# Kernel tuning notes

Hardware: AMD Instinct MI355X
Metric: run time of the kernel (lower is better)

The kernel has to match this reference:

```python
import jax, jax.numpy as jnp
import numpy as np

N_HEADS_ROUTER = 8
N_HEADS_INPUT = 4
LN_EPS = 1e-5

def gelu(x):
    return jax.nn.gelu(x, approximate=False)  # torch F.gelu default (erf)

def mha(x, wq, wk, wv, bq, bk, bv, wo, bo, n_heads):
    # PyTorch nn.MultiheadAttention (batch_first, eval mode)
    B, S, E = x.shape
    d = E // n_heads
    scale = 1.0 / np.sqrt(d).astype(np.float32)
    def split(t):
        return t.reshape(B, S, n_heads, d).transpose(0, 2, 1, 3)  # [B,H,S,d]
    q = split(x @ wq.T + bq)
    k = split(x @ wk.T + bk)
    v = split(x @ wv.T + bv)
    attn = jax.nn.softmax(jnp.einsum('bhqd,bhkd->bhqk', q, k) * scale, axis=-1)
    o = jnp.einsum('bhqk,bhkd->bhqd', attn, v).transpose(0, 2, 1, 3).reshape(B, S, E)
    return o @ wo.T + bo

def layer_norm(x, g, b):
    mu = x.mean(axis=-1, keepdims=True)
    var = ((x - mu) ** 2).mean(axis=-1, keepdims=True)
    return (x - mu) * jax.lax.rsqrt(var + LN_EPS) * g + b

def setup_inputs() -> dict:
    key = jax.random.key(0)
    ks = jax.random.split(key, 20)
    B, S, D, NI, NP = 4, 1024, 1024, 512, 1024
    def rn(k, shape, s=0.02):
        return jax.random.normal(k, shape, jnp.float32) * s
    return {
        'x': jax.random.normal(ks[0], (B, S, D), jnp.float32),
        # DynamicRouter MHA (embed=d_model, 8 heads)
        'r_wq': rn(ks[1], (D, D)), 'r_wk': rn(ks[2], (D, D)), 'r_wv': rn(ks[3], (D, D)),
        'r_bq': jnp.zeros((D,), jnp.float32), 'r_bk': jnp.zeros((D,), jnp.float32), 'r_bv': jnp.zeros((D,), jnp.float32),
        'r_wo': rn(ks[4], (D, D)), 'r_bo': jnp.zeros((D,), jnp.float32),
        'aff_w': rn(ks[5], (NI, D)), 'aff_b': jnp.zeros((NI,), jnp.float32),
        # InputNeurons
        'patterns': rn(ks[6], (NI, D), 0.05),
        'i_wq': rn(ks[7], (NI, NI)), 'i_wk': rn(ks[8], (NI, NI)), 'i_wv': rn(ks[9], (NI, NI)),
        'i_bq': jnp.zeros((NI,), jnp.float32), 'i_bk': jnp.zeros((NI,), jnp.float32), 'i_bv': jnp.zeros((NI,), jnp.float32),
        'i_wo': rn(ks[10], (NI, NI)), 'i_bo': jnp.zeros((NI,), jnp.float32),
        'ln_g': jnp.ones((NI,), jnp.float32), 'ln_b': jnp.zeros((NI,), jnp.float32),
        # ProcessNeurons
        'comb_w': rn(ks[11], (NP, NI), 0.05),
        'proj_w': rn(ks[12], (NP, D), 0.05),
        'k_input': 256,
        'k_process': 512,
    }

def reference(x, r_wq, r_wk, r_wv, r_bq, r_bk, r_bv, r_wo, r_bo, aff_w, aff_b,
              patterns, i_wq, i_wk, i_wv, i_bq, i_bk, i_bv, i_wo, i_bo,
              ln_g, ln_b, comb_w, proj_w, k_input, k_process):
    B, S, D = x.shape
    NI = aff_w.shape[0]
    # --- DynamicRouter ---
    context = mha(x, r_wq, r_wk, r_wv, r_bq, r_bk, r_bv, r_wo, r_bo, N_HEADS_ROUTER)
    affinity = context @ aff_w.T + aff_b           # [B,S,NI]
    scores = affinity.max(axis=1)                  # [B,NI] (max-pool over seq)
    probs = jax.nn.softmax(scores, axis=-1)
    _, idx = jax.lax.top_k(scores, k_input)        # [B,k_in]
    one_hot = jax.nn.one_hot(idx, NI, dtype=probs.dtype).sum(axis=1)  # [B,NI]
    weights = jax.lax.stop_gradient(one_hot - probs) + probs          # straight-through
    # --- InputNeurons ---
    act = gelu(context @ patterns.T)               # [B,S,NI]
    attn_out = mha(act, i_wq, i_wk, i_wv, i_bq, i_bk, i_bv, i_wo, i_bo, N_HEADS_INPUT)
    act = layer_norm(act + attn_out, ln_g, ln_b)
    # --- select input neurons ---
    weighted = act * weights[:, None, :]
    sel = jnp.take_along_axis(weighted, jnp.broadcast_to(idx[:, None, :], (B, S, k_input)), axis=2)  # [B,S,k_in]
    # --- ProcessNeurons ---
    sel_w = comb_w[:, idx].transpose(1, 0, 2)      # [B, NP, k_in]
    pa = gelu(jnp.einsum('bsk,bpk->bsp', sel, sel_w))  # [B,S,NP]
    ps = pa.mean(axis=1)                            # [B,NP]
    _, pidx = jax.lax.top_k(ps, k_process)          # [B,k_p]
    spa = jnp.take_along_axis(pa, jnp.broadcast_to(pidx[:, None, :], (B, S, k_process)), axis=2)  # [B,S,k_p]
    sproj = proj_w[pidx]                            # [B,k_p,D]
    return jnp.einsum('bsk,bkd->bsd', spa, sproj)   # [B,S,D]
```

## Files before the change

kernel.cpp:

```cpp
#include <hip/hip_runtime.h>
#include <math.h>

#define DEVI static __device__ __forceinline__

typedef __attribute__((ext_vector_type(8))) short short8;
typedef __attribute__((ext_vector_type(4))) float f32x4;
typedef unsigned short u16;

DEVI float gelu_f(float x) {
    return 0.5f * x * (1.0f + erff(x * 0.7071067811865475f));
}
DEVI u16 f2bf(float f) {
    unsigned u = __builtin_bit_cast(unsigned, f);
    return (u16)((u + 0x7fffu + ((u >> 16) & 1u)) >> 16);
}
DEVI float bf2f(u16 b) {
    unsigned u = ((unsigned)b) << 16;
    return __builtin_bit_cast(float, u);
}
DEVI void split_bf(float v, u16& h, u16& l) {
    h = f2bf(v);
    l = f2bf(v - bf2f(h));
}

template<int BN, bool SPLIT, bool DO_GELU, int OMODE>
__global__ __launch_bounds__(256, 2)
void gemm_planes(const u16* __restrict__ Agh, const u16* __restrict__ Agl,
                 const u16* __restrict__ Bgh, const u16* __restrict__ Bgl,
                 const float* __restrict__ bias, float* __restrict__ Cf,
                 u16* __restrict__ O1h, u16* __restrict__ O1l,
                 u16* __restrict__ O2h, u16* __restrict__ O2l,
                 u16* __restrict__ O3h, u16* __restrict__ O3l,
                 int M, int N, int K, int HH, int partN)
{
    constexpr int BM = 128, BK = 64, PK = 72;
    constexpr int NPL = SPLIT ? 2 : 1;
    constexpr int MF  = (BN == 128) ? 4 : 2;
    constexpr int NB  = BN / 32;
    __shared__ __align__(16) u16 As[NPL][BM * PK];
    __shared__ __align__(16) u16 Bs[NPL][BN * PK];
    const int t = threadIdx.x, w = t >> 6, l = t & 63;
    const int lr = l & 15, lg = l >> 4;
    const int m0 = blockIdx.y * BM, n0 = blockIdx.x * BN;
    const int moff = (BN == 128) ? (w >> 1) * 64 : w * 32;
    const int noff = (BN == 128) ? (w & 1) * 64 : 0;
    const int srow = t >> 3, sslot = t & 7;

    f32x4 acc[MF][4];
    #pragma unroll
    for (int i = 0; i < MF; ++i)
        #pragma unroll
        for (int j = 0; j < 4; ++j) acc[i][j] = 0.0f;

    for (int k0 = 0; k0 < K; k0 += BK) {
        __syncthreads();
        #pragma unroll
        for (int p = 0; p < 4; ++p) {
            int row = p * 32 + srow;
            size_t g = (size_t)(m0 + row) * K + k0 + sslot * 8;
            *(uint4*)&As[0][row * PK + sslot * 8] = *(const uint4*)&Agh[g];
            if constexpr (SPLIT)
                *(uint4*)&As[1][row * PK + sslot * 8] = *(const uint4*)&Agl[g];
        }
        #pragma unroll
        for (int p = 0; p < NB; ++p) {
            int row = p * 32 + srow;
            size_t g = (size_t)(n0 + row) * K + k0 + sslot * 8;
            *(uint4*)&Bs[0][row * PK + sslot * 8] = *(const uint4*)&Bgh[g];
            if constexpr (SPLIT)
                *(uint4*)&Bs[1][row * PK + sslot * 8] = *(const uint4*)&Bgl[g];
        }
        __syncthreads();
        #pragma unroll
        for (int ks = 0; ks < 2; ++ks) {
            short8 af[MF][NPL], bfr[4][NPL];
            #pragma unroll
            for (int mf = 0; mf < MF; ++mf) {
                int a = (moff + mf * 16 + lr) * PK + ks * 32 + lg * 8;
                af[mf][0] = *(const short8*)&As[0][a];
                if constexpr (SPLIT) af[mf][1] = *(const short8*)&As[1][a];
            }
            #pragma unroll
            for (int nf = 0; nf < 4; ++nf) {
                int a = (noff + nf * 16 + lr) * PK + ks * 32 + lg * 8;
                bfr[nf][0] = *(const short8*)&Bs[0][a];
                if constexpr (SPLIT) bfr[nf][1] = *(const short8*)&Bs[1][a];
            }
            #pragma unroll
            for (int mf = 0; mf < MF; ++mf)
                #pragma unroll
                for (int nf = 0; nf < 4; ++nf) {
                    acc[mf][nf] = __builtin_amdgcn_mfma_f32_16x16x32_bf16(
                        af[mf][0], bfr[nf][0], acc[mf][nf], 0, 0, 0);
                    if constexpr (SPLIT) {
                        acc[mf][nf] = __builtin_amdgcn_mfma_f32_16x16x32_bf16(
                            af[mf][0], bfr[nf][1], acc[mf][nf], 0, 0, 0);
                        acc[mf][nf] = __builtin_amdgcn_mfma_f32_16x16x32_bf16(
                            af[mf][1], bfr[nf][0], acc[mf][nf], 0, 0, 0);
                    }
                }
        }
    }

    float colred[4];
    if constexpr (OMODE == 4) {
        colred[0] = colred[1] = colred[2] = colred[3] = -3.402823466e38f;
    } else if constexpr (OMODE == 5) {
        colred[0] = colred[1] = colred[2] = colred[3] = 0.0f;
    }
    #pragma unroll
    for (int mf = 0; mf < MF; ++mf)
        #pragma unroll
        for (int nf = 0; nf < 4; ++nf) {
            int col  = n0 + noff + nf * 16 + lr;
            int mrow = m0 + moff + mf * 16 + lg * 4;
            float bv = bias ? bias[col] : 0.0f;
            float ov[4];
            #pragma unroll
            for (int r = 0; r < 4; ++r) ov[r] = acc[mf][nf][r] + bv;
            if constexpr (OMODE == 0) {
                #pragma unroll
                for (int r = 0; r < 4; ++r) {
                    float o = ov[r];
                    if constexpr (DO_GELU) o = gelu_f(o);
                    Cf[(size_t)(mrow + r) * N + col] = o;
                }
            } else if constexpr (OMODE == 1) {
                #pragma unroll
                for (int r = 0; r < 4; ++r) {
                    float o = ov[r];
                    if constexpr (DO_GELU) o = gelu_f(o);
                    u16 hb, lb; split_bf(o, hb, lb);
                    O1h[(size_t)(mrow + r) * N + col] = hb;
                    O1l[(size_t)(mrow + r) * N + col] = lb;
                }
            } else if constexpr (OMODE == 3) {
                if (col < partN) {
                    #pragma unroll
                    for (int r = 0; r < 4; ++r) {
                        u16 hb, lb; split_bf(ov[r], hb, lb);
                        O1h[(size_t)(mrow + r) * partN + col] = hb;
                        O1l[(size_t)(mrow + r) * partN + col] = lb;
                    }
                } else if (col < 2 * partN) {
                    int c2 = col - partN;
                    #pragma unroll
                    for (int r = 0; r < 4; ++r) {
                        u16 hb, lb; split_bf(ov[r], hb, lb);
                        O2h[(size_t)(mrow + r) * partN + c2] = hb;
                        O2l[(size_t)(mrow + r) * partN + c2] = lb;
                    }
                } else {
                    int c2 = col - 2 * partN;
                    int hh = c2 >> 7, dd = c2 & 127;
                    int bb = mrow >> 10, s0 = mrow & 1023;
                    size_t idx = ((size_t)(bb * HH + hh) * 128 + dd) * 1024 + s0;
                    ushort4 oh, ol;
                    #pragma unroll
                    for (int r = 0; r < 4; ++r) {
                        u16 hb, lb; split_bf(ov[r], hb, lb);
                        ((u16*)&oh)[r] = hb; ((u16*)&ol)[r] = lb;
                    }
                    *(ushort4*)&O3h[idx] = oh;
                    *(ushort4*)&O3l[idx] = ol;
                }
            } else if constexpr (OMODE == 4) {
                if (n0 < partN) {
                    #pragma unroll
                    for (int r = 0; r < 4; ++r)
                        colred[nf] = fmaxf(colred[nf], ov[r]);
                } else {
                    int c2 = col - partN;
                    #pragma unroll
                    for (int r = 0; r < 4; ++r) {
                        float o = gelu_f(ov[r]);
                        u16 hb, lb; split_bf(o, hb, lb);
                        O1h[(size_t)(mrow + r) * partN + c2] = hb;
                        O1l[(size_t)(mrow + r) * partN + c2] = lb;
                    }
                }
            } else if constexpr (OMODE == 5) {
                #pragma unroll
                for (int r = 0; r < 4; ++r) {
                    float o = gelu_f(ov[r]);
                    colred[nf] += o;
                    u16 hb, lb; split_bf(o, hb, lb);
                    O1h[(size_t)(mrow + r) * N + col] = hb;
                    O1l[(size_t)(mrow + r) * N + col] = lb;
                }
            }
        }
    if constexpr (OMODE == 4 || OMODE == 5) {
        bool doRed = (OMODE == 5) || (n0 < partN);
        if (doRed) {
            __syncthreads();
            float* sred = (float*)&As[0][0];
            #pragma unroll
            for (int nf = 0; nf < 4; ++nf) sred[t * 4 + nf] = colred[nf];
            __syncthreads();
            if (t < 128) {
                int cl = t, lrr = cl & 15, nff = (cl & 63) >> 4, wb = cl >> 6;
                float a = (OMODE == 4) ? -3.402823466e38f : 0.0f;
                #pragma unroll
                for (int k2 = 0; k2 < 2; ++k2)
                    #pragma unroll
                    for (int l2 = 0; l2 < 4; ++l2) {
                        float v = sred[(((wb + 2 * k2) * 64) + l2 * 16 + lrr) * 4 + nff];
                        if constexpr (OMODE == 4) a = fmaxf(a, v); else a += v;
                    }
                int stride = (OMODE == 4) ? partN : N;
                Cf[(size_t)blockIdx.y * stride + n0 + cl] = a;
            }
        }
    }
}

__global__ __launch_bounds__(256, 3)
void attn_planes(const u16* __restrict__ Qh, const u16* __restrict__ Ql,
                 const u16* __restrict__ Kh, const u16* __restrict__ Kl,
                 const u16* __restrict__ Vh, const u16* __restrict__ Vl,
                 u16* __restrict__ Oh, u16* __restrict__ Ol,
                 int S, int Dm, int H, float scale)
{
    __shared__ __align__(16) u16 KsL[2][32 * 136];
    __shared__ __align__(16) u16 VsL[2][128 * 40];
    __shared__ __align__(16) u16 PsL[2][4 * 16 * 40];
    const int t = threadIdx.x, w = t >> 6, l = t & 63;
    const int lr = l & 15, lg = l >> 4;
    const int nqt = gridDim.x;
    const int nwg = nqt * gridDim.y;
    const int fid = blockIdx.y * nqt + blockIdx.x;
    const int nid = (fid & 7) * (nwg >> 3) + (fid >> 3);
    const int bh = nid / nqt, qt = nid - bh * nqt;
    const int b = bh / H, h = bh - b * H;
    const int q0 = qt * 64 + w * 16;
    const size_t qkbase = (size_t)(b * S) * Dm + h * 128;
    const size_t vbase  = (size_t)(b * H + h) * 128 * 1024;

    short8 qhf[4], qlf[4];
    #pragma unroll
    for (int ks = 0; ks < 4; ++ks) {
        size_t g = qkbase + (size_t)(q0 + lr) * Dm + ks * 32 + lg * 8;
        qhf[ks] = *(const short8*)&Qh[g];
        qlf[ks] = *(const short8*)&Ql[g];
    }
    f32x4 accO[8];
    #pragma unroll
    for (int i = 0; i < 8; ++i) accO[i] = 0.0f;
    float ls = 0.0f;
    const int pw = w * 640;

    for (int c0 = 0; c0 < S; c0 += 32) {
        __syncthreads();
        #pragma unroll
        for (int p = 0; p < 2; ++p) {
            int key = p * 16 + (t >> 4);
            int slot = t & 15;
            size_t g = qkbase + (size_t)(c0 + key) * Dm + slot * 8;
            *(uint4*)&KsL[0][key * 136 + slot * 8] = *(const uint4*)&Kh[g];
            *(uint4*)&KsL[1][key * 136 + slot * 8] = *(const uint4*)&Kl[g];
        }
        #pragma unroll
        for (int p = 0; p < 2; ++p) {
            int d = p * 64 + (t >> 2);
            int ksl = t & 3;
            size_t g = vbase + (size_t)d * 1024 + c0 + ksl * 8;
            *(uint4*)&VsL[0][d * 40 + ksl * 8] = *(const uint4*)&Vh[g];
            *(uint4*)&VsL[1][d * 40 + ksl * 8] = *(const uint4*)&Vl[g];
        }
        __syncthreads();
        f32x4 sac[2];
        sac[0] = 0.0f; sac[1] = 0.0f;
        #pragma unroll
        for (int mt = 0; mt < 2; ++mt)
            #pragma unroll
            for (int ks = 0; ks < 4; ++ks) {
                int a = (mt * 16 + lr) * 136 + ks * 32 + lg * 8;
                short8 khf = *(const short8*)&KsL[0][a];
                short8 klf = *(const short8*)&KsL[1][a];
                sac[mt] = __builtin_amdgcn_mfma_f32_16x16x32_bf16(khf, qhf[ks], sac[mt], 0, 0, 0);
                sac[mt] = __builtin_amdgcn_mfma_f32_16x16x32_bf16(khf, qlf[ks], sac[mt], 0, 0, 0);
                sac[mt] = __builtin_amdgcn_mfma_f32_16x16x32_bf16(klf, qhf[ks], sac[mt], 0, 0, 0);
            }
        #pragma unroll
        for (int mt = 0; mt < 2; ++mt)
            #pragma unroll
            for (int rr = 0; rr < 4; ++rr) {
                float p = __expf(sac[mt][rr] * scale);
                ls += p;
                int key = mt * 16 + lg * 4 + rr;
                u16 hb, lb; split_bf(p, hb, lb);
                PsL[0][pw + lr * 40 + key] = hb;
                PsL[1][pw + lr * 40 + key] = lb;
            }
        short8 pah = *(const short8*)&PsL[0][pw + lr * 40 + lg * 8];
        short8 pal = *(const short8*)&PsL[1][pw + lr * 40 + lg * 8];
        #pragma unroll
        for (int nt = 0; nt < 8; ++nt) {
            int a = (nt * 16 + lr) * 40 + lg * 8;
            short8 vhf = *(const short8*)&VsL[0][a];
            short8 vlf = *(const short8*)&VsL[1][a];
            accO[nt] = __builtin_amdgcn_mfma_f32_16x16x32_bf16(pah, vhf, accO[nt], 0, 0, 0);
            accO[nt] = __builtin_amdgcn_mfma_f32_16x16x32_bf16(pah, vlf, accO[nt], 0, 0, 0);
            accO[nt] = __builtin_amdgcn_mfma_f32_16x16x32_bf16(pal, vhf, accO[nt], 0, 0, 0);
        }
    }
    float lt = ls + __shfl_xor(ls, 16, 64);
    lt += __shfl_xor(lt, 32, 64);
    #pragma unroll
    for (int rr = 0; rr < 4; ++rr) {
        float inv = 1.0f / __shfl(lt, lg * 4 + rr, 64);
        size_t rowoff = qkbase + (size_t)(q0 + lg * 4 + rr) * Dm;
        #pragma unroll
        for (int nt = 0; nt < 8; ++nt) {
            float o = accO[nt][rr] * inv;
            u16 hb, lb; split_bf(o, hb, lb);
            Oh[rowoff + nt * 16 + lr] = hb;
            Ol[rowoff + nt * 16 + lr] = lb;
        }
    }
}

struct PSeg { const float* s; u16* h; u16* l; int n4; int pad; };
struct PArgs { PSeg g[8]; };

__global__ __launch_bounds__(256)
void pack_many(PArgs a)
{
    PSeg sg = a.g[blockIdx.y];
    int i = blockIdx.x * 256 + threadIdx.x;
    if (i >= sg.n4) return;
    float4 v = *(const float4*)&sg.s[i * 4];
    ushort4 hv, lv;
    split_bf(v.x, hv.x, lv.x);
    split_bf(v.y, hv.y, lv.y);
    split_bf(v.z, hv.z, lv.z);
    split_bf(v.w, hv.w, lv.w);
    *(ushort4*)&sg.h[i * 4] = hv;
    *(ushort4*)&sg.l[i * 4] = lv;
}

__global__ __launch_bounds__(256)
void pack_f32(const float* __restrict__ src, u16* __restrict__ dh,
              u16* __restrict__ dl, int n4)
{
    int i = blockIdx.x * 256 + threadIdx.x;
    if (i >= n4) return;
    float4 v = *(const float4*)&src[i * 4];
    ushort4 hv, lv;
    split_bf(v.x, hv.x, lv.x);
    split_bf(v.y, hv.y, lv.y);
    split_bf(v.z, hv.z, lv.z);
    split_bf(v.w, hv.w, lv.w);
    *(ushort4*)&dh[i * 4] = hv;
    *(ushort4*)&dl[i * 4] = lv;
}

__global__ __launch_bounds__(256)
void packT64(const float* __restrict__ src, u16* __restrict__ dh,
             u16* __restrict__ dl, int R, int C)
{
    __shared__ float tile[64][65];
    int r0 = blockIdx.y * 64, c0 = blockIdx.x * 64;
    int t = threadIdx.x;
    #pragma unroll
    for (int i = 0; i < 16; ++i) {
        int idx = i * 256 + t, rr = idx >> 6, cc = idx & 63;
        tile[rr][cc] = src[(size_t)(r0 + rr) * C + c0 + cc];
    }
    __syncthreads();
    #pragma unroll
    for (int i = 0; i < 16; ++i) {
        int idx = i * 256 + t, rr = idx >> 6, cc = idx & 63;
        float v = tile[cc][rr];
        u16 hb, lb; split_bf(v, hb, lb);
        size_t o = (size_t)(c0 + rr) * R + r0 + cc;
        dh[o] = hb; dl[o] = lb;
    }
}

__global__ __launch_bounds__(1024)
void concat_bias(const float* rq, const float* rk, const float* rv,
                 const float* iq, const float* ik, const float* iv,
                 const float* ab, float* rb, float* ib, float* apb)
{
    int t = threadIdx.x;
    rb[t]        = rq[t];
    rb[1024 + t] = rk[t];
    rb[2048 + t] = rv[t];
    apb[t] = (t < 512) ? ab[t] : 0.0f;
    if (t < 512) {
        ib[t]        = iq[t];
        ib[512 + t]  = ik[t];
        ib[1024 + t] = iv[t];
    }
}

__global__ __launch_bounds__(256)
void mask_rows(u16* __restrict__ ph, const float* __restrict__ mask)
{
    int i = blockIdx.x * 256 + threadIdx.x;
    int i4 = i * 4;
    int bb = i4 >> 20;
    int col = i4 & 1023;
    ushort4 v = *(ushort4*)&ph[i4];
    float4 m = *(const float4*)&mask[bb * 1024 + col];
    if (m.x == 0.f) v.x = 0;
    if (m.y == 0.f) v.y = 0;
    if (m.z == 0.f) v.z = 0;
    if (m.w == 0.f) v.w = 0;
    *(ushort4*)&ph[i4] = v;
}

template<int OP>
__global__ __launch_bounds__(256)
void reduce8(const float* __restrict__ P, float* __restrict__ Y, int N, float scl)
{
    int n = blockIdx.x * 256 + threadIdx.x;
    int b = blockIdx.y;
    float a = (OP == 0) ? -3.402823466e38f : 0.0f;
    #pragma unroll
    for (int r = 0; r < 8; ++r) {
        float v = P[(size_t)(b * 8 + r) * N + n];
        if (OP == 0) a = fmaxf(a, v); else a += v;
    }
    Y[(size_t)b * N + n] = (OP == 0) ? a : a * scl;
}

template<int N, int KSEL>
__global__ __launch_bounds__(1024)
void topk_mask_kernel(const float* __restrict__ Sc, float* __restrict__ mask)
{
    __shared__ float v[N];
    __shared__ int   id[N];
    int t = threadIdx.x;
    int b = blockIdx.x;
    v[t]  = Sc[b * N + t];
    id[t] = t;
    __syncthreads();
    for (int k = 2; k <= N; k <<= 1) {
        for (int j = k >> 1; j > 0; j >>= 1) {
            int ixj = t ^ j;
            if (ixj > t) {
                bool dir = ((t & k) == 0);
                float va = v[t], vb = v[ixj];
                int   ia = id[t], ib = id[ixj];
                bool before_b = (vb > va) || (vb == va && ib < ia);
                bool sw = dir ? before_b : !before_b;
                if (sw) { v[t] = vb; v[ixj] = va; id[t] = ib; id[ixj] = ia; }
            }
            __syncthreads();
        }
    }
    mask[b * N + id[t]] = (t < KSEL) ? 1.0f : 0.0f;
}

__global__ __launch_bounds__(256)
void ln_mask_planes(const u16* __restrict__ Xh, const u16* __restrict__ Xl,
                    const u16* __restrict__ Rh, const u16* __restrict__ Rl,
                    const float* __restrict__ gam, const float* __restrict__ bet,
                    const float* __restrict__ mask,
                    u16* __restrict__ Yh, u16* __restrict__ Yl)
{
    int row = blockIdx.x, bb = row >> 10, t = threadIdx.x;
    size_t base = (size_t)row * 512;
    float a1 = bf2f(Xh[base + t]) + bf2f(Xl[base + t])
             + bf2f(Rh[base + t]) + bf2f(Rl[base + t]);
    float a2 = bf2f(Xh[base + t + 256]) + bf2f(Xl[base + t + 256])
             + bf2f(Rh[base + t + 256]) + bf2f(Rl[base + t + 256]);
    float s  = a1 + a2;
    float sq = a1 * a1 + a2 * a2;
    #pragma unroll
    for (int off = 32; off > 0; off >>= 1) {
        s  += __shfl_down(s, off, 64);
        sq += __shfl_down(sq, off, 64);
    }
    __shared__ float red[8];
    int wid = t >> 6, lane = t & 63;
    if (lane == 0) { red[wid] = s; red[wid + 4] = sq; }
    __syncthreads();
    if (t == 0) {
        float st  = red[0] + red[1] + red[2] + red[3];
        float sqt = red[4] + red[5] + red[6] + red[7];
        float mu  = st / 512.0f;
        float var = sqt / 512.0f - mu * mu;
        red[0] = mu;
        red[1] = rsqrtf(var + 1e-5f);
    }
    __syncthreads();
    float mu = red[0], rstd = red[1];
    float y1 = ((a1 - mu) * rstd * gam[t] + bet[t]) * mask[bb * 512 + t];
    float y2 = ((a2 - mu) * rstd * gam[t + 256] + bet[t + 256]) * mask[bb * 512 + t + 256];
    u16 hb, lb;
    split_bf(y1, hb, lb); Yh[base + t] = hb;       Yl[base + t] = lb;
    split_bf(y2, hb, lb); Yh[base + t + 256] = hb; Yl[base + t + 256] = lb;
}

extern "C" void kernel_launch(void* const* d_in, const int* in_sizes, int n_in,
                              void* d_out, int out_size, void* d_ws, size_t ws_size,
                              hipStream_t stream)
{
    (void)in_sizes; (void)n_in; (void)out_size; (void)ws_size;
    const float* x        = (const float*)d_in[0];
    const float* r_wq     = (const float*)d_in[1];
    const float* r_wk     = (const float*)d_in[2];
    const float* r_wv     = (const float*)d_in[3];
    const float* r_bq     = (const float*)d_in[4];
    const float* r_bk     = (const float*)d_in[5];
    const float* r_bv     = (const float*)d_in[6];
    const float* r_wo     = (const float*)d_in[7];
    const float* r_bo     = (const float*)d_in[8];
    const float* aff_w    = (const float*)d_in[9];
    const float* aff_b    = (const float*)d_in[10];
    const float* patterns = (const float*)d_in[11];
    const float* i_wq     = (const float*)d_in[12];
    const float* i_wk     = (const float*)d_in[13];
    const float* i_wv     = (const float*)d_in[14];
    const float* i_bq     = (const float*)d_in[15];
    const float* i_bk     = (const float*)d_in[16];
    const float* i_bv     = (const float*)d_in[17];
    const float* i_wo     = (const float*)d_in[18];
    const float* i_bo     = (const float*)d_in[19];
    const float* ln_g     = (const float*)d_in[20];
    const float* ln_b     = (const float*)d_in[21];
    const float* comb_w   = (const float*)d_in[22];
    const float* proj_w   = (const float*)d_in[23];

    constexpr size_t MBy = 1024 * 1024;
    char* base = (char*)d_ws;

    u16* xh   = (u16*)(base);             u16* xl   = (u16*)(base + 8 * MBy);
    u16* aph  = xh;                        u16* apl  = xl;
    u16* cbh  = (u16*)(base);             u16* cbl  = (u16*)(base + 1 * MBy);
    u16* pjh  = (u16*)(base + 2 * MBy);   u16* pjl  = (u16*)(base + 4 * MBy);
    u16* acth = (u16*)(base + 8 * MBy);   u16* actl = (u16*)(base + 12 * MBy);
    u16* rqh  = (u16*)(base + 16 * MBy);  u16* rql  = (u16*)(base + 24 * MBy);
    u16* ctxh = rqh;                       u16* ctxl = rql;
    u16* pah  = rqh;                       u16* pal  = rql;
    u16* rkh  = (u16*)(base + 32 * MBy);  u16* rkl  = (u16*)(base + 40 * MBy);
    u16* iqh  = (u16*)(base + 32 * MBy);  u16* iql  = (u16*)(base + 36 * MBy);
    u16* ikh  = (u16*)(base + 40 * MBy);  u16* ikl  = (u16*)(base + 44 * MBy);
    u16* a2fh = iqh;                       u16* a2fl = iql;
    u16* lnmh = ikh;                       u16* lnml = ikl;
    u16* rvth = (u16*)(base + 48 * MBy);  u16* rvtl = (u16*)(base + 56 * MBy);
    u16* ivth = (u16*)(base + 48 * MBy);  u16* ivtl = (u16*)(base + 52 * MBy);
    u16* a2ph = (u16*)(base + 56 * MBy);  u16* a2pl = (u16*)(base + 60 * MBy);
    u16* wqkvh  = (u16*)(base + 64 * MBy); u16* wqkvl = (u16*)(base + 70 * MBy);
    u16* woh    = (u16*)(base + 64 * MBy); u16* wol   = (u16*)(base + 66 * MBy);
    u16* apbh   = (u16*)(base + 68 * MBy); u16* apbl  = (u16*)(base + 70 * MBy);
    u16* iwqkvh = (u16*)(base + 72 * MBy);
    u16* iwqkvl = (u16*)(base + 72 * MBy + 1572864);
    u16* iwoh   = (u16*)(base + 75 * MBy);
    u16* iwol   = (u16*)(base + 75 * MBy + 524288);
    float* partial = (float*)(base + 76 * MBy);
    float* scores  = (float*)(base + 76 * MBy + 262144);
    float* maskI   = scores + 2048;
    float* ps      = maskI + 2048;
    float* maskP   = ps + 4096;
    float* rbias   = maskP + 4096;
    float* ibias   = rbias + 3072;
    float* apbias  = ibias + 1536;

    const float scale = 0.08838834764831843f;
    dim3 blk(256);

    concat_bias<<<dim3(1), dim3(1024), 0, stream>>>(r_bq, r_bk, r_bv,
        i_bq, i_bk, i_bv, aff_b, rbias, ibias, apbias);
    {
        PArgs a{};
        a.g[0] = {x,    xh,              xl,              1048576, 0};
        a.g[1] = {r_wq, wqkvh,           wqkvl,           262144,  0};
        a.g[2] = {r_wk, wqkvh + 1048576, wqkvl + 1048576, 262144,  0};
        a.g[3] = {r_wv, wqkvh + 2097152, wqkvl + 2097152, 262144,  0};
        pack_many<<<dim3(4096, 4), blk, 0, stream>>>(a);
    }

    gemm_planes<128, true, false, 3><<<dim3(24, 32), blk, 0, stream>>>(
        xh, xl, wqkvh, wqkvl, rbias, nullptr,
        rqh, rql, rkh, rkl, rvth, rvtl, 4096, 3072, 1024, 8, 1024);

    {
        PArgs a{};
        a.g[0] = {r_wo,     woh,             wol,             262144, 0};
        a.g[1] = {aff_w,    apbh,            apbl,            131072, 0};
        a.g[2] = {patterns, apbh + 524288,   apbl + 524288,   131072, 0};
        a.g[3] = {i_wq,     iwqkvh,          iwqkvl,          65536,  0};
        a.g[4] = {i_wk,     iwqkvh + 262144, iwqkvl + 262144, 65536,  0};
        a.g[5] = {i_wv,     iwqkvh + 524288, iwqkvl + 524288, 65536,  0};
        a.g[6] = {i_wo,     iwoh,            iwol,            65536,  0};
        pack_many<<<dim3(1024, 7), blk, 0, stream>>>(a);
    }

    attn_planes<<<dim3(16, 32), blk, 0, stream>>>(rqh, rql, rkh, rkl, rvth, rvtl,
                                                  aph, apl, 1024, 1024, 8, scale);
    gemm_planes<128, true, false, 1><<<dim3(8, 32), blk, 0, stream>>>(
        aph, apl, woh, wol, r_bo, nullptr,
        ctxh, ctxl, nullptr, nullptr, nullptr, nullptr, 4096, 1024, 1024, 0, 0);

    gemm_planes<128, true, false, 4><<<dim3(8, 32), blk, 0, stream>>>(
        ctxh, ctxl, apbh, apbl, apbias, partial,
        acth, actl, nullptr, nullptr, nullptr, nullptr, 4096, 1024, 1024, 0, 512);
    reduce8<0><<<dim3(2, 4), blk, 0, stream>>>(partial, scores, 512, 1.0f);
    topk_mask_kernel<512, 256><<<dim3(4), dim3(512), 0, stream>>>(scores, maskI);

    pack_f32<<<512, blk, 0, stream>>>(comb_w, cbh, cbl, 131072);
    packT64<<<dim3(16, 16), blk, 0, stream>>>(proj_w, pjh, pjl, 1024, 1024);

    gemm_planes<128, true, false, 3><<<dim3(12, 32), blk, 0, stream>>>(
        acth, actl, iwqkvh, iwqkvl, ibias, nullptr,
        iqh, iql, ikh, ikl, ivth, ivtl, 4096, 1536, 512, 4, 512);
    attn_planes<<<dim3(16, 16), blk, 0, stream>>>(iqh, iql, ikh, ikl, ivth, ivtl,
                                                  a2ph, a2pl, 1024, 512, 4, scale);
    gemm_planes<64, true, false, 1><<<dim3(8, 32), blk, 0, stream>>>(
        a2ph, a2pl, iwoh, iwol, i_bo, nullptr,
        a2fh, a2fl, nullptr, nullptr, nullptr, nullptr, 4096, 512, 512, 0, 0);
    ln_mask_planes<<<dim3(4096), blk, 0, stream>>>(acth, actl, a2fh, a2fl,
                                                   ln_g, ln_b, maskI, lnmh, lnml);

    gemm_planes<128, true, true, 5><<<dim3(8, 32), blk, 0, stream>>>(
        lnmh, lnml, cbh, cbl, nullptr, partial,
        pah, pal, nullptr, nullptr, nullptr, nullptr, 4096, 1024, 512, 0, 0);
    reduce8<1><<<dim3(4, 4), blk, 0, stream>>>(partial, ps, 1024, 1.0f / 1024.0f);
    topk_mask_kernel<1024, 512><<<dim3(4), dim3(1024), 0, stream>>>(ps, maskP);
    mask_rows<<<4096, blk, 0, stream>>>(pah, maskP);

    gemm_planes<128, false, false, 0><<<dim3(8, 32), blk, 0, stream>>>(
        pah, nullptr, pjh, nullptr, nullptr, (float*)d_out,
        nullptr, nullptr, nullptr, nullptr, nullptr, nullptr, 4096, 1024, 1024, 0, 0);
}
```

Before: 492.7 us.

## Fuse partial reduction into rank-based top-k and shrink second attention blocks

Replaces the separate reduce8 and bitonic-sort top-k kernels with a single kernel that reduces the 8 partials and computes each element's rank by an O(N) scan over shared memory. This removes two launches and the many syncthreads-bound bitonic stages. Separately, attention is templated on waves per block, and the input-neuron attention (only 4 heads) runs with 2-wave blocks and twice as many blocks to raise occupancy across CUs. The rank scan costs O(N^2) total comparisons, and mean scaling is dropped, which leaves the top-k ordering unchanged.

After: 524.3 us. 1.06x slower.

```diff
diff --git a/kernel.cpp b/kernel.cpp
--- a/kernel.cpp
+++ b/kernel.cpp
@@ -215,16 +215,19 @@
     }
 }
 
-__global__ __launch_bounds__(256, 3)
+template<int NW>
+__global__ __launch_bounds__(NW * 64, (NW == 4) ? 3 : 2)
 void attn_planes(const u16* __restrict__ Qh, const u16* __restrict__ Ql,
                  const u16* __restrict__ Kh, const u16* __restrict__ Kl,
                  const u16* __restrict__ Vh, const u16* __restrict__ Vl,
                  u16* __restrict__ Oh, u16* __restrict__ Ol,
                  int S, int Dm, int H, float scale)
 {
+    constexpr int NT = NW * 64;
+    constexpr int KIT = 512 / NT;
     __shared__ __align__(16) u16 KsL[2][32 * 136];
     __shared__ __align__(16) u16 VsL[2][128 * 40];
-    __shared__ __align__(16) u16 PsL[2][4 * 16 * 40];
+    __shared__ __align__(16) u16 PsL[2][NW * 16 * 40];
     const int t = threadIdx.x, w = t >> 6, l = t & 63;
     const int lr = l & 15, lg = l >> 4;
     const int nqt = gridDim.x;
@@ -233,7 +236,7 @@
     const int nid = (fid & 7) * (nwg >> 3) + (fid >> 3);
     const int bh = nid / nqt, qt = nid - bh * nqt;
     const int b = bh / H, h = bh - b * H;
-    const int q0 = qt * 64 + w * 16;
+    const int q0 = qt * (NW * 16) + w * 16;
     const size_t qkbase = (size_t)(b * S) * Dm + h * 128;
     const size_t vbase  = (size_t)(b * H + h) * 128 * 1024;
 
@@ -253,17 +256,17 @@
     for (int c0 = 0; c0 < S; c0 += 32) {
         __syncthreads();
         #pragma unroll
-        for (int p = 0; p < 2; ++p) {
-            int key = p * 16 + (t >> 4);
-            int slot = t & 15;
+        for (int p = 0; p < KIT; ++p) {
+            int idx = p * NT + t;
+            int key = idx >> 4, slot = idx & 15;
             size_t g = qkbase + (size_t)(c0 + key) * Dm + slot * 8;
             *(uint4*)&KsL[0][key * 136 + slot * 8] = *(const uint4*)&Kh[g];
             *(uint4*)&KsL[1][key * 136 + slot * 8] = *(const uint4*)&Kl[g];
         }
         #pragma unroll
-        for (int p = 0; p < 2; ++p) {
-            int d = p * 64 + (t >> 2);
-            int ksl = t & 3;
+        for (int p = 0; p < KIT; ++p) {
+            int idx = p * NT + t;
+            int d = idx >> 2, ksl = idx & 3;
             size_t g = vbase + (size_t)d * 1024 + c0 + ksl * 8;
             *(uint4*)&VsL[0][d * 40 + ksl * 8] = *(const uint4*)&Vh[g];
             *(uint4*)&VsL[1][d * 40 + ksl * 8] = *(const uint4*)&Vl[g];
@@ -412,47 +415,26 @@
     *(ushort4*)&ph[i4] = v;
 }
 
-template<int OP>
-__global__ __launch_bounds__(256)
-void reduce8(const float* __restrict__ P, float* __restrict__ Y, int N, float scl)
-{
-    int n = blockIdx.x * 256 + threadIdx.x;
-    int b = blockIdx.y;
+template<int N, int KSEL, int OP>
+__global__ __launch_bounds__(1024)
+void topk_rank(const float* __restrict__ P, float* __restrict__ mask)
+{
+    __shared__ float v[N];
+    int t = threadIdx.x, b = blockIdx.x;
     float a = (OP == 0) ? -3.402823466e38f : 0.0f;
     #pragma unroll
     for (int r = 0; r < 8; ++r) {
-        float v = P[(size_t)(b * 8 + r) * N + n];
-        if (OP == 0) a = fmaxf(a, v); else a += v;
-    }
-    Y[(size_t)b * N + n] = (OP == 0) ? a : a * scl;
-}
-
-template<int N, int KSEL>
-__global__ __launch_bounds__(1024)
-void topk_mask_kernel(const float* __restrict__ Sc, float* __restrict__ mask)
-{
-    __shared__ float v[N];
-    __shared__ int   id[N];
-    int t = threadIdx.x;
-    int b = blockIdx.x;
-    v[t]  = Sc[b * N + t];
-    id[t] = t;
+        float x = P[(size_t)(b * 8 + r) * N + t];
+        if (OP == 0) a = fmaxf(a, x); else a += x;
+    }
+    v[t] = a;
     __syncthreads();
-    for (int k = 2; k <= N; k <<= 1) {
-        for (int j = k >> 1; j > 0; j >>= 1) {
-            int ixj = t ^ j;
-            if (ixj > t) {
-                bool dir = ((t & k) == 0);
-                float va = v[t], vb = v[ixj];
-                int   ia = id[t], ib = id[ixj];
-                bool before_b = (vb > va) || (vb == va && ib < ia);
-                bool sw = dir ? before_b : !before_b;
-                if (sw) { v[t] = vb; v[ixj] = va; id[t] = ib; id[ixj] = ia; }
-            }
-            __syncthreads();
-        }
-    }
-    mask[b * N + id[t]] = (t < KSEL) ? 1.0f : 0.0f;
+    int rank = 0;
+    for (int j = 0; j < N; ++j) {
+        float vj = v[j];
+        rank += (vj > a) || (vj == a && j < t);
+    }
+    mask[b * N + t] = (rank < KSEL) ? 1.0f : 0.0f;
 }
 
 __global__ __launch_bounds__(256)
@@ -553,10 +535,8 @@
     u16* iwoh   = (u16*)(base + 75 * MBy);
     u16* iwol   = (u16*)(base + 75 * MBy + 524288);
     float* partial = (float*)(base + 76 * MBy);
-    float* scores  = (float*)(base + 76 * MBy + 262144);
-    float* maskI   = scores + 2048;
-    float* ps      = maskI + 2048;
-    float* maskP   = ps + 4096;
+    float* maskI   = (float*)(base + 76 * MBy + 262144);
+    float* maskP   = maskI + 2048;
     float* rbias   = maskP + 4096;
     float* ibias   = rbias + 3072;
     float* apbias  = ibias + 1536;
@@ -591,8 +571,8 @@
         pack_many<<<dim3(1024, 7), blk, 0, stream>>>(a);
     }
 
-    attn_planes<<<dim3(16, 32), blk, 0, stream>>>(rqh, rql, rkh, rkl, rvth, rvtl,
-                                                  aph, apl, 1024, 1024, 8, scale);
+    attn_planes<4><<<dim3(16, 32), dim3(256), 0, stream>>>(
+        rqh, rql, rkh, rkl, rvth, rvtl, aph, apl, 1024, 1024, 8, scale);
     gemm_planes<128, true, false, 1><<<dim3(8, 32), blk, 0, stream>>>(
         aph, apl, woh, wol, r_bo, nullptr,
         ctxh, ctxl, nullptr, nullptr, nullptr, nullptr, 4096, 1024, 1024, 0, 0);
@@ -600,8 +580,7 @@
     gemm_planes<128, true, false, 4><<<dim3(8, 32), blk, 0, stream>>>(
         ctxh, ctxl, apbh, apbl, apbias, partial,
         acth, actl, nullptr, nullptr, nullptr, nullptr, 4096, 1024, 1024, 0, 512);
-    reduce8<0><<<dim3(2, 4), blk, 0, stream>>>(partial, scores, 512, 1.0f);
-    topk_mask_kernel<512, 256><<<dim3(4), dim3(512), 0, stream>>>(scores, maskI);
+    topk_rank<512, 256, 0><<<dim3(4), dim3(512), 0, stream>>>(partial, maskI);
 
     pack_f32<<<512, blk, 0, stream>>>(comb_w, cbh, cbl, 131072);
     packT64<<<dim3(16, 16), blk, 0, stream>>>(proj_w, pjh, pjl, 1024, 1024);
@@ -609,8 +588,8 @@
     gemm_planes<128, true, false, 3><<<dim3(12, 32), blk, 0, stream>>>(
         acth, actl, iwqkvh, iwqkvl, ibias, nullptr,
         iqh, iql, ikh, ikl, ivth, ivtl, 4096, 1536, 512, 4, 512);
-    attn_planes<<<dim3(16, 16), blk, 0, stream>>>(iqh, iql, ikh, ikl, ivth, ivtl,
-                                                  a2ph, a2pl, 1024, 512, 4, scale);
+    attn_planes<2><<<dim3(32, 16), dim3(128), 0, stream>>>(
+        iqh, iql, ikh, ikl, ivth, ivtl, a2ph, a2pl, 1024, 512, 4, scale);
     gemm_planes<64, true, false, 1><<<dim3(8, 32), blk, 0, stream>>>(
         a2ph, a2pl, iwoh, iwol, i_bo, nullptr,
         a2fh, a2fl, nullptr, nullptr, nullptr, nullptr, 4096, 512, 512, 0, 0);
@@ -620,8 +599,7 @@
     gemm_planes<128, true, true, 5><<<dim3(8, 32), blk, 0, stream>>>(
         lnmh, lnml, cbh, cbl, nullptr, partial,
         pah, pal, nullptr, nullptr, nullptr, nullptr, 4096, 1024, 512, 0, 0);
-    reduce8<1><<<dim3(4, 4), blk, 0, stream>>>(partial, ps, 1024, 1.0f / 1024.0f);
-    topk_mask_kernel<1024, 512><<<dim3(4), dim3(1024), 0, stream>>>(ps, maskP);
+    topk_rank<1024, 512, 1><<<dim3(4), dim3(1024), 0, stream>>>(partial, maskP);
     mask_rows<<<4096, blk, 0, stream>>>(pah, maskP);
 
     gemm_planes<128, false, false, 0><<<dim3(8, 32), blk, 0, stream>>>(
```
